# Optimization experiments

Hardware: AMD Instinct MI355X
Metric: run time of the kernel (lower is better)

The kernel has to match this reference:

```python
import jax, jax.numpy as jnp
import numpy as np

N_BATCHES = 32
N_LABELS = 100


def setup_inputs() -> dict:
    key = jax.random.key(0)
    ks = jax.random.split(key, 7)
    N, D, P = 16384, 2048, 256
    x = jax.random.normal(ks[0], (N, D), dtype=jnp.float32)
    label = jax.random.randint(ks[1], (N,), 0, N_LABELS, dtype=jnp.int64)
    label_batch = jnp.sort(jax.random.randint(ks[2], (N,), 0, N_BATCHES, dtype=jnp.int64))
    W1_w = jax.random.normal(ks[3], (P, D), dtype=jnp.float32) * 0.02
    W1_b = jax.random.normal(ks[4], (P,), dtype=jnp.float32) * 0.02
    W2_w = jax.random.normal(ks[5], (P, D), dtype=jnp.float32) * 0.02
    W2_b = jax.random.normal(ks[6], (P,), dtype=jnp.float32) * 0.02
    return {"x": x, "label": label, "label_batch": label_batch,
            "W1_w": W1_w, "W1_b": W1_b, "W2_w": W2_w, "W2_b": W2_b}


def _loo_diff_label_mean(x, label, label_batch):
    # For each sample i: mean of x over {j : label_batch[j]==label_batch[i] and label[j]!=label[i]}.
    # Rows with no such j are zero (torch code's `continue`). x is detached in the original.
    N = x.shape[0]
    xs = jax.lax.stop_gradient(x)
    seg = label_batch * N_LABELS + label                      # combined (group,label) key
    n_seg = N_BATCHES * N_LABELS
    ones = jnp.ones((N,), dtype=x.dtype)
    sum_bl = jax.ops.segment_sum(xs, seg, num_segments=n_seg)            # [n_seg, D]
    cnt_bl = jax.ops.segment_sum(ones, seg, num_segments=n_seg)          # [n_seg]
    sum_b = jax.ops.segment_sum(xs, label_batch, num_segments=N_BATCHES)  # [NB, D]
    cnt_b = jax.ops.segment_sum(ones, label_batch, num_segments=N_BATCHES)
    diff_sum = sum_b[label_batch] - sum_bl[seg]               # [N, D]
    diff_cnt = cnt_b[label_batch] - cnt_bl[seg]               # [N]
    safe = jnp.maximum(diff_cnt, 1.0)
    mean = diff_sum / safe[:, None]
    return jnp.where((diff_cnt > 0)[:, None], mean, jnp.zeros_like(mean))


def reference(x, label, label_batch, W1_w, W1_b, W2_w, W2_b):
    calc_mean = _loo_diff_label_mean(x, label, label_batch)   # detached aggregate
    return x @ W1_w.T + W1_b + calc_mean @ W2_w.T + W2_b      # W1(x) + W2(mean)
```

## Files before the change

### kernel.cpp

```cpp
#include <hip/hip_runtime.h>
#include <cstdint>

#define N_SAMPLES 16384
#define DIM 2048
#define PDIM 256
#define NB 32
#define NL 100
#define NSEG (NB * NL)

typedef float floatx4 __attribute__((ext_vector_type(4)));
typedef __bf16 bf16x8 __attribute__((ext_vector_type(8)));

__device__ __forceinline__ unsigned short f32_to_bf16(float f) {
    unsigned int u = __float_as_uint(f);
    u += 0x7fffu + ((u >> 16) & 1u);
    return (unsigned short)(u >> 16);
}
__device__ __forceinline__ unsigned int pack_bf16x2(float a, float b) {
    return (unsigned int)f32_to_bf16(a) | ((unsigned int)f32_to_bf16(b) << 16);
}

__global__ __launch_bounds__(256) void prep_kernel(
    const float* __restrict__ W1w, const float* __restrict__ W1b,
    const float* __restrict__ W2w, const float* __restrict__ W2b,
    const int* __restrict__ label, const int* __restrict__ lbatch,
    unsigned short* __restrict__ Wbf, float* __restrict__ bias,
    int* __restrict__ seg, int* __restrict__ cnt, float* __restrict__ SW2)
{
    int i = blockIdx.x * 256 + threadIdx.x;
    Wbf[i]              = f32_to_bf16(W1w[i]);
    Wbf[PDIM * DIM + i] = f32_to_bf16(W2w[i]);
    if (i < PDIM) bias[i] = W1b[i] + W2b[i];
    if (i < N_SAMPLES) seg[i] = lbatch[i] * NL + label[i];
    if (i < NSEG) cnt[i] = 0;
    if (i < NSEG * PDIM / 2) ((float2*)SW2)[i] = make_float2(0.f, 0.f);
}

__global__ __launch_bounds__(256) void hist_kernel(
    const int* __restrict__ seg, int* __restrict__ cnt)
{
    int i = blockIdx.x * 256 + threadIdx.x;
    atomicAdd(&cnt[seg[i]], 1);
}

__global__ __launch_bounds__(256) void gemm_fused_kernel(
    const float* __restrict__ x, const unsigned short* __restrict__ Wbf,
    const float* __restrict__ bias, const int* __restrict__ seg,
    float* __restrict__ out, float* __restrict__ SW2)
{
    constexpr int BM = 64, BN = 256, BK = 32;
    __shared__ __align__(16) unsigned short ldsA[BM * BK];
    __shared__ __align__(16) unsigned short ldsB[BN * BK];
    const int tid = threadIdx.x;
    const int lane = tid & 63;
    const int wave = tid >> 6;
    const int quad = lane >> 4, l15 = lane & 15;
    const int nhalf = blockIdx.x;
    const int m0 = blockIdx.y * BM;
    const int srow = lane >> 2, schunk = lane & 3;
    const int arow = tid >> 2;
    const int akc = (tid & 3) * 8;

    floatx4 acc[4][4];
    #pragma unroll
    for (int i = 0; i < 4; ++i)
        #pragma unroll
        for (int j = 0; j < 4; ++j) acc[i][j] = (floatx4){0.f, 0.f, 0.f, 0.f};

    const float* Ax = x + (size_t)(m0 + arow) * DIM + akc;
    const unsigned short* Bbase =
        Wbf + ((size_t)(nhalf * BN) + srow) * DIM + schunk * 8;

    for (int kk = 0; kk < DIM; kk += BK) {
        float4 a0 = *(const float4*)(Ax + kk);
        float4 a1 = *(const float4*)(Ax + kk + 4);
        __syncthreads();
        uint4 ao;
        ao.x = pack_bf16x2(a0.x, a0.y);
        ao.y = pack_bf16x2(a0.z, a0.w);
        ao.z = pack_bf16x2(a1.x, a1.y);
        ao.w = pack_bf16x2(a1.z, a1.w);
        *(uint4*)&ldsA[arow * BK + akc] = ao;
        #pragma unroll
        for (int ch = wave; ch < BN / 16; ch += 4)
            __builtin_amdgcn_global_load_lds(
                (const __attribute__((address_space(1))) void*)(Bbase + (size_t)ch * 16 * DIM + kk),
                (__attribute__((address_space(3))) void*)&ldsB[ch * 16 * BK], 16, 0, 0);
        __syncthreads();

        bf16x8 af[4], bf[4];
        #pragma unroll
        for (int mi = 0; mi < 4; ++mi)
            af[mi] = *(const bf16x8*)&ldsA[(mi * 16 + l15) * BK + quad * 8];
        #pragma unroll
        for (int ni = 0; ni < 4; ++ni)
            bf[ni] = *(const bf16x8*)&ldsB[(wave * 64 + ni * 16 + l15) * BK + quad * 8];
        #pragma unroll
        for (int mi = 0; mi < 4; ++mi)
            #pragma unroll
            for (int ni = 0; ni < 4; ++ni)
                acc[mi][ni] = __builtin_amdgcn_mfma_f32_16x16x32_bf16(
                    af[mi], bf[ni], acc[mi][ni], 0, 0, 0);
    }

    if (nhalf == 0) {
        #pragma unroll
        for (int mi = 0; mi < 4; ++mi) {
            const int rbase = m0 + mi * 16 + quad * 4;
            #pragma unroll
            for (int ni = 0; ni < 4; ++ni) {
                const int col = wave * 64 + ni * 16 + l15;
                const float bs = bias[col];
                #pragma unroll
                for (int r = 0; r < 4; ++r)
                    out[(size_t)(rbase + r) * PDIM + col] = acc[mi][ni][r] + bs;
            }
        }
    } else {
        #pragma unroll
        for (int mi = 0; mi < 4; ++mi) {
            const int rbase = m0 + mi * 16 + quad * 4;
            #pragma unroll
            for (int r = 0; r < 4; ++r) {
                const int sr = seg[rbase + r];
                #pragma unroll
                for (int ni = 0; ni < 4; ++ni) {
                    const int col = wave * 64 + ni * 16 + l15;
                    atomicAdd(&SW2[(size_t)sr * PDIM + col], acc[mi][ni][r]);
                }
            }
        }
    }
}

__global__ __launch_bounds__(256) void finalize_kernel(
    float* __restrict__ SW2, const int* __restrict__ cnt)
{
    const int b = blockIdx.x;
    const int col = threadIdx.x;
    int cb = 0;
    #pragma unroll 4
    for (int l = 0; l < NL; ++l) cb += cnt[b * NL + l];
    float tot = 0.f;
    #pragma unroll 4
    for (int l = 0; l < NL; ++l)
        tot += SW2[(size_t)(b * NL + l) * PDIM + col];
    for (int l = 0; l < NL; ++l) {
        const int s = b * NL + l;
        const int dc = cb - cnt[s];
        const float v = SW2[(size_t)s * PDIM + col];
        SW2[(size_t)s * PDIM + col] = (dc > 0) ? (tot - v) / (float)dc : 0.f;
    }
}

__global__ __launch_bounds__(256) void epilogue_kernel(
    float* __restrict__ out, const float* __restrict__ SW2,
    const int* __restrict__ seg)
{
    const int idx = blockIdx.x * 256 + threadIdx.x;
    const int row = idx >> 6;
    const int c = (idx & 63) * 4;
    float4 v = ((const float4*)out)[idx];
    const float4 s4 = *(const float4*)&SW2[(size_t)seg[row] * PDIM + c];
    v.x += s4.x; v.y += s4.y; v.z += s4.z; v.w += s4.w;
    ((float4*)out)[idx] = v;
}

extern "C" void kernel_launch(void* const* d_in, const int* in_sizes, int n_in,
                              void* d_out, int out_size, void* d_ws, size_t ws_size,
                              hipStream_t stream)
{
    const float* x      = (const float*)d_in[0];
    const int*   label  = (const int*)d_in[1];
    const int*   lbatch = (const int*)d_in[2];
    const float* W1w    = (const float*)d_in[3];
    const float* W1b    = (const float*)d_in[4];
    const float* W2w    = (const float*)d_in[5];
    const float* W2b    = (const float*)d_in[6];
    float* out = (float*)d_out;

    char* ws = (char*)d_ws;
    size_t off = 0;
    auto alloc = [&](size_t bytes) {
        void* p = ws + off;
        off = (off + bytes + 255) & ~(size_t)255;
        return p;
    };
    unsigned short* Wbf = (unsigned short*)alloc((size_t)2 * PDIM * DIM * 2);
    float* SW2  = (float*)alloc((size_t)NSEG * PDIM * 4);
    float* bias = (float*)alloc(PDIM * 4);
    int*   seg  = (int*)alloc(N_SAMPLES * 4);
    int*   cnt  = (int*)alloc(NSEG * 4);

    prep_kernel<<<PDIM * DIM / 256, 256, 0, stream>>>(
        W1w, W1b, W2w, W2b, label, lbatch, Wbf, bias, seg, cnt, SW2);

    hist_kernel<<<N_SAMPLES / 256, 256, 0, stream>>>(seg, cnt);

    gemm_fused_kernel<<<dim3(2, N_SAMPLES / 64), 256, 0, stream>>>(
        x, Wbf, bias, seg, out, SW2);

    finalize_kernel<<<NB, 256, 0, stream>>>(SW2, cnt);

    epilogue_kernel<<<(size_t)N_SAMPLES * PDIM / 4 / 256, 256, 0, stream>>>(
        out, SW2, seg);
}
```

Before: 298.1 us.

## Split-K GEMM by two, prefetch A tile, and swizzle LDS A layout

```diff
diff --git a/kernel.cpp b/kernel.cpp
--- a/kernel.cpp
+++ b/kernel.cpp
@@ -45,10 +45,11 @@
 
 __global__ __launch_bounds__(256) void gemm_fused_kernel(
     const float* __restrict__ x, const unsigned short* __restrict__ Wbf,
-    const float* __restrict__ bias, const int* __restrict__ seg,
-    float* __restrict__ out, float* __restrict__ SW2)
-{
-    constexpr int BM = 64, BN = 256, BK = 32;
+    const int* __restrict__ seg,
+    float* __restrict__ outp,
+    float* __restrict__ SW2)
+{
+    constexpr int BM = 64, BN = 256, BK = 32, KS = 2;
     __shared__ __align__(16) unsigned short ldsA[BM * BK];
     __shared__ __align__(16) unsigned short ldsB[BN * BK];
     const int tid = threadIdx.x;
@@ -57,9 +58,14 @@
     const int quad = lane >> 4, l15 = lane & 15;
     const int nhalf = blockIdx.x;
     const int m0 = blockIdx.y * BM;
+    const int z = blockIdx.z;
+    const int k0 = z * (DIM / KS);
+    const int nt = (DIM / KS) / BK;
     const int srow = lane >> 2, schunk = lane & 3;
     const int arow = tid >> 2;
-    const int akc = (tid & 3) * 8;
+    const int acol = tid & 3;
+    const int aslot_w = acol ^ ((arow ^ (arow >> 2)) & 3);
+    const int aslot_r = quad ^ ((l15 ^ (l15 >> 2)) & 3);
 
     floatx4 acc[4][4];
     #pragma unroll
@@ -67,31 +73,37 @@
         #pragma unroll
         for (int j = 0; j < 4; ++j) acc[i][j] = (floatx4){0.f, 0.f, 0.f, 0.f};
 
-    const float* Ax = x + (size_t)(m0 + arow) * DIM + akc;
+    const float* Ax = x + (size_t)(m0 + arow) * DIM + acol * 8;
     const unsigned short* Bbase =
         Wbf + ((size_t)(nhalf * BN) + srow) * DIM + schunk * 8;
 
-    for (int kk = 0; kk < DIM; kk += BK) {
-        float4 a0 = *(const float4*)(Ax + kk);
-        float4 a1 = *(const float4*)(Ax + kk + 4);
+    float4 a0 = *(const float4*)(Ax + k0);
+    float4 a1 = *(const float4*)(Ax + k0 + 4);
+
+    for (int t = 0; t < nt; ++t) {
+        const int kk = k0 + t * BK;
         __syncthreads();
         uint4 ao;
         ao.x = pack_bf16x2(a0.x, a0.y);
         ao.y = pack_bf16x2(a0.z, a0.w);
         ao.z = pack_bf16x2(a1.x, a1.y);
         ao.w = pack_bf16x2(a1.z, a1.w);
-        *(uint4*)&ldsA[arow * BK + akc] = ao;
+        *(uint4*)&ldsA[arow * BK + aslot_w * 8] = ao;
         #pragma unroll
         for (int ch = wave; ch < BN / 16; ch += 4)
             __builtin_amdgcn_global_load_lds(
                 (const __attribute__((address_space(1))) void*)(Bbase + (size_t)ch * 16 * DIM + kk),
                 (__attribute__((address_space(3))) void*)&ldsB[ch * 16 * BK], 16, 0, 0);
+        if (t + 1 < nt) {
+            a0 = *(const float4*)(Ax + kk + BK);
+            a1 = *(const float4*)(Ax + kk + BK + 4);
+        }
         __syncthreads();
 
         bf16x8 af[4], bf[4];
         #pragma unroll
         for (int mi = 0; mi < 4; ++mi)
-            af[mi] = *(const bf16x8*)&ldsA[(mi * 16 + l15) * BK + quad * 8];
+            af[mi] = *(const bf16x8*)&ldsA[(mi * 16 + l15) * BK + aslot_r * 8];
         #pragma unroll
         for (int ni = 0; ni < 4; ++ni)
             bf[ni] = *(const bf16x8*)&ldsB[(wave * 64 + ni * 16 + l15) * BK + quad * 8];
@@ -104,16 +116,16 @@
     }
 
     if (nhalf == 0) {
+        float* op = outp + (size_t)z * N_SAMPLES * PDIM;
         #pragma unroll
         for (int mi = 0; mi < 4; ++mi) {
             const int rbase = m0 + mi * 16 + quad * 4;
             #pragma unroll
             for (int ni = 0; ni < 4; ++ni) {
                 const int col = wave * 64 + ni * 16 + l15;
-                const float bs = bias[col];
                 #pragma unroll
                 for (int r = 0; r < 4; ++r)
-                    out[(size_t)(rbase + r) * PDIM + col] = acc[mi][ni][r] + bs;
+                    op[(size_t)(rbase + r) * PDIM + col] = acc[mi][ni][r];
             }
         }
     } else {
@@ -154,16 +166,23 @@
 }
 
 __global__ __launch_bounds__(256) void epilogue_kernel(
-    float* __restrict__ out, const float* __restrict__ SW2,
+    float* __restrict__ out, const float* __restrict__ outp,
+    const float* __restrict__ SW2, const float* __restrict__ bias,
     const int* __restrict__ seg)
 {
     const int idx = blockIdx.x * 256 + threadIdx.x;
     const int row = idx >> 6;
     const int c = (idx & 63) * 4;
-    float4 v = ((const float4*)out)[idx];
+    float4 v0 = ((const float4*)outp)[idx];
+    float4 v1 = ((const float4*)outp)[idx + N_SAMPLES * PDIM / 4];
+    const float4 b4 = *(const float4*)&bias[c];
     const float4 s4 = *(const float4*)&SW2[(size_t)seg[row] * PDIM + c];
-    v.x += s4.x; v.y += s4.y; v.z += s4.z; v.w += s4.w;
-    ((float4*)out)[idx] = v;
+    float4 o;
+    o.x = v0.x + v1.x + b4.x + s4.x;
+    o.y = v0.y + v1.y + b4.y + s4.y;
+    o.z = v0.z + v1.z + b4.z + s4.z;
+    o.w = v0.w + v1.w + b4.w + s4.w;
+    ((float4*)out)[idx] = o;
 }
 
 extern "C" void kernel_launch(void* const* d_in, const int* in_sizes, int n_in,
@@ -186,6 +205,7 @@
         off = (off + bytes + 255) & ~(size_t)255;
         return p;
     };
+    float* outp = (float*)alloc((size_t)2 * N_SAMPLES * PDIM * 4);
     unsigned short* Wbf = (unsigned short*)alloc((size_t)2 * PDIM * DIM * 2);
     float* SW2  = (float*)alloc((size_t)NSEG * PDIM * 4);
     float* bias = (float*)alloc(PDIM * 4);
@@ -197,11 +217,11 @@
 
     hist_kernel<<<N_SAMPLES / 256, 256, 0, stream>>>(seg, cnt);
 
-    gemm_fused_kernel<<<dim3(2, N_SAMPLES / 64), 256, 0, stream>>>(
-        x, Wbf, bias, seg, out, SW2);
+    gemm_fused_kernel<<<dim3(2, N_SAMPLES / 64, 2), 256, 0, stream>>>(
+        x, Wbf, seg, outp, SW2);
 
     finalize_kernel<<<NB, 256, 0, stream>>>(SW2, cnt);
 
     epilogue_kernel<<<(size_t)N_SAMPLES * PDIM / 4 / 256, 256, 0, stream>>>(
-        out, SW2, seg);
-}
+        out, outp, SW2, bias, seg);
+}
```

Result: slower. 331.3 us (+11.1%).

## Pre-convert x to bf16 and retile GEMM to 128x128 blocks with async LDS loads

Applied to the files above, without the earlier changes.

```diff
diff --git a/kernel.cpp b/kernel.cpp
--- a/kernel.cpp
+++ b/kernel.cpp
@@ -43,23 +43,37 @@
     atomicAdd(&cnt[seg[i]], 1);
 }
 
-__global__ __launch_bounds__(256) void gemm_fused_kernel(
-    const float* __restrict__ x, const unsigned short* __restrict__ Wbf,
+__global__ __launch_bounds__(256) void xconv_kernel(
+    const float* __restrict__ x, unsigned short* __restrict__ xb)
+{
+    const size_t idx = (size_t)blockIdx.x * 256 + threadIdx.x;
+    const float4 a0 = *(const float4*)(x + idx * 8);
+    const float4 a1 = *(const float4*)(x + idx * 8 + 4);
+    uint4 o;
+    o.x = pack_bf16x2(a0.x, a0.y);
+    o.y = pack_bf16x2(a0.z, a0.w);
+    o.z = pack_bf16x2(a1.x, a1.y);
+    o.w = pack_bf16x2(a1.z, a1.w);
+    *(uint4*)(xb + idx * 8) = o;
+}
+
+__global__ __launch_bounds__(256) void gemm512_kernel(
+    const unsigned short* __restrict__ A,
+    const unsigned short* __restrict__ Wbf,
     const float* __restrict__ bias, const int* __restrict__ seg,
     float* __restrict__ out, float* __restrict__ SW2)
 {
-    constexpr int BM = 64, BN = 256, BK = 32;
+    constexpr int BM = 128, BN = 128, BK = 32;
     __shared__ __align__(16) unsigned short ldsA[BM * BK];
     __shared__ __align__(16) unsigned short ldsB[BN * BK];
     const int tid = threadIdx.x;
     const int lane = tid & 63;
     const int wave = tid >> 6;
+    const int wr = wave >> 1, wc = wave & 1;
     const int quad = lane >> 4, l15 = lane & 15;
-    const int nhalf = blockIdx.x;
-    const int m0 = blockIdx.y * BM;
+    const int m0 = blockIdx.x * BM;
+    const int n0 = blockIdx.y * BN;
     const int srow = lane >> 2, schunk = lane & 3;
-    const int arow = tid >> 2;
-    const int akc = (tid & 3) * 8;
 
     floatx4 acc[4][4];
     #pragma unroll
@@ -67,20 +81,16 @@
         #pragma unroll
         for (int j = 0; j < 4; ++j) acc[i][j] = (floatx4){0.f, 0.f, 0.f, 0.f};
 
-    const float* Ax = x + (size_t)(m0 + arow) * DIM + akc;
-    const unsigned short* Bbase =
-        Wbf + ((size_t)(nhalf * BN) + srow) * DIM + schunk * 8;
+    const unsigned short* Abase = A + (size_t)(m0 + srow) * DIM + schunk * 8;
+    const unsigned short* Bbase = Wbf + (size_t)(n0 + srow) * DIM + schunk * 8;
 
     for (int kk = 0; kk < DIM; kk += BK) {
-        float4 a0 = *(const float4*)(Ax + kk);
-        float4 a1 = *(const float4*)(Ax + kk + 4);
         __syncthreads();
-        uint4 ao;
-        ao.x = pack_bf16x2(a0.x, a0.y);
-        ao.y = pack_bf16x2(a0.z, a0.w);
-        ao.z = pack_bf16x2(a1.x, a1.y);
-        ao.w = pack_bf16x2(a1.z, a1.w);
-        *(uint4*)&ldsA[arow * BK + akc] = ao;
+        #pragma unroll
+        for (int ch = wave; ch < BM / 16; ch += 4)
+            __builtin_amdgcn_global_load_lds(
+                (const __attribute__((address_space(1))) void*)(Abase + (size_t)ch * 16 * DIM + kk),
+                (__attribute__((address_space(3))) void*)&ldsA[ch * 16 * BK], 16, 0, 0);
         #pragma unroll
         for (int ch = wave; ch < BN / 16; ch += 4)
             __builtin_amdgcn_global_load_lds(
@@ -91,10 +101,10 @@
         bf16x8 af[4], bf[4];
         #pragma unroll
         for (int mi = 0; mi < 4; ++mi)
-            af[mi] = *(const bf16x8*)&ldsA[(mi * 16 + l15) * BK + quad * 8];
+            af[mi] = *(const bf16x8*)&ldsA[(wr * 64 + mi * 16 + l15) * BK + quad * 8];
         #pragma unroll
         for (int ni = 0; ni < 4; ++ni)
-            bf[ni] = *(const bf16x8*)&ldsB[(wave * 64 + ni * 16 + l15) * BK + quad * 8];
+            bf[ni] = *(const bf16x8*)&ldsB[(wc * 64 + ni * 16 + l15) * BK + quad * 8];
         #pragma unroll
         for (int mi = 0; mi < 4; ++mi)
             #pragma unroll
@@ -103,13 +113,13 @@
                     af[mi], bf[ni], acc[mi][ni], 0, 0, 0);
     }
 
-    if (nhalf == 0) {
+    if (n0 < PDIM) {
         #pragma unroll
         for (int mi = 0; mi < 4; ++mi) {
-            const int rbase = m0 + mi * 16 + quad * 4;
+            const int rbase = m0 + wr * 64 + mi * 16 + quad * 4;
             #pragma unroll
             for (int ni = 0; ni < 4; ++ni) {
-                const int col = wave * 64 + ni * 16 + l15;
+                const int col = n0 + wc * 64 + ni * 16 + l15;
                 const float bs = bias[col];
                 #pragma unroll
                 for (int r = 0; r < 4; ++r)
@@ -117,15 +127,16 @@
             }
         }
     } else {
+        const int c0 = n0 - PDIM;
         #pragma unroll
         for (int mi = 0; mi < 4; ++mi) {
-            const int rbase = m0 + mi * 16 + quad * 4;
+            const int rbase = m0 + wr * 64 + mi * 16 + quad * 4;
             #pragma unroll
             for (int r = 0; r < 4; ++r) {
                 const int sr = seg[rbase + r];
                 #pragma unroll
                 for (int ni = 0; ni < 4; ++ni) {
-                    const int col = wave * 64 + ni * 16 + l15;
+                    const int col = c0 + wc * 64 + ni * 16 + l15;
                     atomicAdd(&SW2[(size_t)sr * PDIM + col], acc[mi][ni][r]);
                 }
             }
@@ -186,6 +197,7 @@
         off = (off + bytes + 255) & ~(size_t)255;
         return p;
     };
+    unsigned short* xb  = (unsigned short*)alloc((size_t)N_SAMPLES * DIM * 2);
     unsigned short* Wbf = (unsigned short*)alloc((size_t)2 * PDIM * DIM * 2);
     float* SW2  = (float*)alloc((size_t)NSEG * PDIM * 4);
     float* bias = (float*)alloc(PDIM * 4);
@@ -197,8 +209,10 @@
 
     hist_kernel<<<N_SAMPLES / 256, 256, 0, stream>>>(seg, cnt);
 
-    gemm_fused_kernel<<<dim3(2, N_SAMPLES / 64), 256, 0, stream>>>(
-        x, Wbf, bias, seg, out, SW2);
+    xconv_kernel<<<(size_t)N_SAMPLES * DIM / 8 / 256, 256, 0, stream>>>(x, xb);
+
+    gemm512_kernel<<<dim3(N_SAMPLES / 128, 4), 256, 0, stream>>>(
+        xb, Wbf, bias, seg, out, SW2);
 
     finalize_kernel<<<NB, 256, 0, stream>>>(SW2, cnt);
 
```

Result: slower. 305.2 us (+2.4%).
